# Performance work log

Hardware: AMD Instinct MI355X
Metric: run time of the kernel (lower is better)

## Reference

```python
import jax, jax.numpy as jnp
import numpy as np

B, N, H, V, STEP = 16, 50, 128, 40000, 2

def setup_inputs() -> dict:
    key = jax.random.key(0)
    ks = jax.random.split(key, 24)
    def nrm(i, shape, s=0.08):
        return jax.random.normal(ks[i], shape, jnp.float32) * s
    items = jax.random.randint(ks[0], (B, N), 0, V)
    A = jax.random.uniform(ks[1], (B, N, 2 * N), jnp.float32)
    lengths = jax.random.randint(ks[2], (B,), 1, N + 1)
    mask = (jnp.arange(N)[None, :] < lengths[:, None]).astype(jnp.int32)
    emb = nrm(3, (V, H), 0.1).at[0].set(0.0)  # padding_idx=0 row zeroed
    return dict(
        items=items, A=A, mask=mask, emb=emb,
        w_ih=nrm(4, (3 * H, 2 * H)), w_hh=nrm(5, (3 * H, H)),
        b_ih=nrm(6, (3 * H,)), b_hh=nrm(7, (3 * H,)),
        b_iah=nrm(8, (H,)), b_oah=nrm(9, (H,)),
        W_ein=nrm(10, (H, H)), b_ein=nrm(11, (H,)),
        W_eout=nrm(12, (H, H)), b_eout=nrm(13, (H,)),
        W_one=nrm(14, (H, H)), b_one=nrm(15, (H,)),
        W_two=nrm(16, (H, H)), b_two=nrm(17, (H,)),
        w_three=nrm(18, (H,)),
        W_tr=nrm(19, (H, 2 * H)), b_tr=nrm(20, (H,)),
        W_t=nrm(21, (H, H)),
    )

def gnn_cell(A, hidden, w_ih, w_hh, b_ih, b_hh, b_iah, b_oah, W_ein, b_ein, W_eout, b_eout):
    # A: [B,N,2N], hidden: [B,N,H]
    ein = hidden @ W_ein.T + b_ein
    eout = hidden @ W_eout.T + b_eout
    input_in = jnp.einsum('bnm,bmh->bnh', A[:, :, :N], ein) + b_iah
    input_out = jnp.einsum('bnm,bmh->bnh', A[:, :, N:], eout) + b_oah
    inputs = jnp.concatenate([input_in, input_out], axis=-1)  # [B,N,2H]
    gi = inputs @ w_ih.T + b_ih
    gh = hidden @ w_hh.T + b_hh
    i_r, i_i, i_n = jnp.split(gi, 3, axis=-1)
    h_r, h_i, h_n = jnp.split(gh, 3, axis=-1)
    resetgate = jax.nn.sigmoid(i_r + h_r)
    inputgate = jax.nn.sigmoid(i_i + h_i)
    newgate = jnp.tanh(i_n + resetgate * h_n)
    return newgate + inputgate * (hidden - newgate)

def reference(items, A, mask, emb, w_ih, w_hh, b_ih, b_hh, b_iah, b_oah,
              W_ein, b_ein, W_eout, b_eout, W_one, b_one, W_two, b_two,
              w_three, W_tr, b_tr, W_t):
    hidden = emb[items]  # [B,N,H]
    for _ in range(STEP):
        hidden = gnn_cell(A, hidden, w_ih, w_hh, b_ih, b_hh, b_iah, b_oah,
                          W_ein, b_ein, W_eout, b_eout)
    # compute_scores
    lengths = jnp.sum(mask, axis=1)  # all >= 1 by construction
    ht = hidden[jnp.arange(B), lengths - 1]  # [B,H] last valid item
    q1 = (ht @ W_one.T + b_one)[:, None, :]
    q2 = hidden @ W_two.T + b_two
    mexp = mask[..., None].astype(jnp.float32)  # [B,N,1]
    alpha_logits = jax.nn.sigmoid(q1 + q2) @ w_three[:, None]  # [B,N,1]
    alpha = jax.nn.softmax(jnp.where(mexp == 0, -jnp.inf, alpha_logits), axis=1)
    a = jnp.sum(alpha * hidden * mexp, axis=1)  # [B,H]
    a = jnp.concatenate([a, ht], axis=1) @ W_tr.T + b_tr  # hybrid (nonhybrid=False)
    b_emb = emb[1:]  # [V-1,H]
    qt = (hidden * mexp) @ W_t.T  # [B,N,H]
    beta_logits = jnp.einsum('vh,bnh->bvn', b_emb, qt)
    beta_logits = jnp.where(mask[:, None, :] == 0, -jnp.inf, beta_logits)
    beta = jax.nn.softmax(beta_logits, axis=-1)  # [B,V-1,N]
    target = jnp.einsum('bvn,bnh->bvh', beta, qt * mexp)  # [B,V-1,H]
    # scores = sum((a[:,None,:] + target) * b_emb, -1), split to avoid extra buffer
    scores = jnp.einsum('bvh,vh->bv', target, b_emb) + a @ b_emb.T
    return scores  # [B, V-1]
```

## Files before the change

kernel.cpp:

```cpp
#include <hip/hip_runtime.h>

#define BB 16
#define NN 50
#define HH 128
#define VV 40000
#define VO 39999

typedef unsigned short u16;
typedef unsigned int u32;
typedef __attribute__((ext_vector_type(8))) short short8;
typedef __attribute__((ext_vector_type(4))) float f32x4;

#define OFF_HID    0
#define OFF_EIN    102400
#define OFF_Q2     102400
#define OFF_EOUT   204800
#define OFF_Q1     204800
#define OFF_HT     206848
#define OFF_QTBF   307200
#define OFF_LEN    411648
#define OFF_WIHT   411664
#define OFF_WHHT   509968
#define OFF_WEINT  559120
#define OFF_WEOUTT 575504
#define OFF_WTWOT  591888
#define OFF_WTT    608272
#define OFF_WONET  624656
#define OFF_WTRT   641040

__device__ __forceinline__ float sigm(float x){ return 1.0f/(1.0f+__expf(-x)); }
__device__ __forceinline__ float b2f(u16 u){
  union { u32 i; float f; } c; c.i = ((u32)u) << 16; return c.f;
}
__device__ __forceinline__ u16 f2b(float f){
  union { float f; u32 i; } c; c.f = f;
  u32 u = c.i;
  return (u16)((u + 0x7fffu + ((u >> 16) & 1u)) >> 16);
}
__device__ __forceinline__ int frag_idx(int b, int n, int k){
  int tile = n>>4, vlo = n&15, kc = k>>5, quad = (k>>3)&3, j = k&7;
  return (((b*4+tile)*4+kc)<<9) + ((quad<<4)+vlo)*8 + j;
}

__global__ void k_pre(const int* __restrict__ items, const float* __restrict__ emb,
                      const float* __restrict__ w_ih, const float* __restrict__ w_hh,
                      const float* __restrict__ W_ein, const float* __restrict__ W_eout,
                      const float* __restrict__ W_two, const float* __restrict__ W_t,
                      const float* __restrict__ W_one, const float* __restrict__ W_tr,
                      float* __restrict__ ws){
  int idx = blockIdx.x*256 + threadIdx.x;
  if (idx < 102400){
    int r = idx >> 7, h = idx & 127;
    ws[OFF_HID + idx] = emb[items[r]*128 + h];
  } else if (idx < 200704){
    int i = idx-102400; int k=i/384, j=i-k*384;
    ws[OFF_WIHT + i] = w_ih[j*256 + k];
  } else if (idx < 249856){
    int i = idx-200704; int k=i/384, j=i-k*384;
    ws[OFF_WHHT + i] = w_hh[j*128 + k];
  } else if (idx < 266240){
    int i = idx-249856; int k=i>>7, h=i&127;
    ws[OFF_WEINT + i] = W_ein[h*128 + k];
  } else if (idx < 282624){
    int i = idx-266240; int k=i>>7, h=i&127;
    ws[OFF_WEOUTT + i] = W_eout[h*128 + k];
  } else if (idx < 299008){
    int i = idx-282624; int k=i>>7, h=i&127;
    ws[OFF_WTWOT + i] = W_two[h*128 + k];
  } else if (idx < 315392){
    int i = idx-299008; int k=i>>7, h=i&127;
    ws[OFF_WTT + i] = W_t[h*128 + k];
  } else if (idx < 331776){
    int i = idx-315392; int k=i>>7, h=i&127;
    ws[OFF_WONET + i] = W_one[h*128 + k];
  } else if (idx < 364544){
    int i = idx-331776; int k=i>>7, h=i&127;
    ws[OFF_WTRT + i] = W_tr[h*256 + k];
  }
}

__global__ void __launch_bounds__(256) k_einout(const float* __restrict__ b_ein,
                         const float* __restrict__ b_eout, float* __restrict__ ws){
  __shared__ float hl[256];
  int t = threadIdx.x;
  int r0 = blockIdx.x * 2;
  hl[t] = ws[OFF_HID + r0*128 + t];
  __syncthreads();
  int h = t & 127;
  const float* wT = ws + ((t<128) ? OFF_WEINT : OFF_WEOUTT);
  float bias = ((t<128)? b_ein : b_eout)[h];
  float a0 = bias, a1 = bias;
  for (int k=0;k<128;k+=4){
    float w0 = wT[(k+0)*128+h], w1 = wT[(k+1)*128+h];
    float w2 = wT[(k+2)*128+h], w3 = wT[(k+3)*128+h];
    float4 h0 = *(const float4*)(hl + k);
    float4 h1 = *(const float4*)(hl + 128 + k);
    a0 += h0.x*w0 + h0.y*w1 + h0.z*w2 + h0.w*w3;
    a1 += h1.x*w0 + h1.y*w1 + h1.z*w2 + h1.w*w3;
  }
  float* dst = ws + ((t<128) ? OFF_EIN : OFF_EOUT);
  dst[(r0+0)*128 + h] = a0;
  dst[(r0+1)*128 + h] = a1;
}

__global__ void __launch_bounds__(384) k_cell(const float* __restrict__ A,
                       const float* __restrict__ b_iah, const float* __restrict__ b_oah,
                       const float* __restrict__ b_ih, const float* __restrict__ b_hh,
                       float* __restrict__ ws){
  __shared__ float hidr[4][128];
  __shared__ float arow[4][104];
  __shared__ float inp[4][256];
  __shared__ float gil[4][384];
  __shared__ float ghl[4][384];
  int t = threadIdx.x;
  int tile = blockIdx.x, b = blockIdx.y;
  int n0 = tile*4;
  for (int o=t; o<512; o+=384){
    int r=o>>7, h=o&127, row=n0+r;
    hidr[r][h] = (row<NN) ? ws[OFF_HID + (b*NN+row)*128 + h] : 0.0f;
  }
  for (int o=t; o<416; o+=384){
    int r=o/104, c=o-r*104;
    arow[r][c] = (c<100 && n0+r<NN) ? A[(size_t)(b*NN+n0+r)*100 + c] : 0.0f;
  }
  __syncthreads();
  for (int o=t; o<1024; o+=384){
    int r = o>>8, c8 = o&255;
    int half = (c8 < 128) ? 1 : 0;
    int c = c8 & 127;
    int row = n0 + r;
    float acc = 0.0f;
    if (row < NN){
      acc = half ? b_iah[c] : b_oah[c];
      const float* src = ws + (half?OFF_EIN:OFF_EOUT) + b*6400 + c;
      const float* ar = &arow[r][half?0:50];
      #pragma unroll 5
      for (int m=0;m<50;m++) acc += ar[m] * src[m*128];
    }
    inp[r][c8] = acc;
  }
  __syncthreads();
  {
    int j = t;
    float gi[4], gh[4];
    float bi = b_ih[j], bh = b_hh[j];
    #pragma unroll
    for (int r=0;r<4;r++){ gi[r]=bi; gh[r]=bh; }
    const float* wti = ws + OFF_WIHT;
    const float* wth = ws + OFF_WHHT;
    for (int k=0;k<256;k+=4){
      float w0 = wti[(k+0)*384+j], w1 = wti[(k+1)*384+j];
      float w2 = wti[(k+2)*384+j], w3_ = wti[(k+3)*384+j];
      #pragma unroll
      for (int r=0;r<4;r++){
        float4 iv = *(const float4*)(&inp[r][k]);
        gi[r] += iv.x*w0 + iv.y*w1 + iv.z*w2 + iv.w*w3_;
      }
    }
    for (int k=0;k<128;k+=4){
      float w0 = wth[(k+0)*384+j], w1 = wth[(k+1)*384+j];
      float w2 = wth[(k+2)*384+j], w3_ = wth[(k+3)*384+j];
      #pragma unroll
      for (int r=0;r<4;r++){
        float4 hv = *(const float4*)(&hidr[r][k]);
        gh[r] += hv.x*w0 + hv.y*w1 + hv.z*w2 + hv.w*w3_;
      }
    }
    #pragma unroll
    for (int r=0;r<4;r++){ gil[r][j]=gi[r]; ghl[r][j]=gh[r]; }
  }
  __syncthreads();
  for (int o=t; o<512; o+=384){
    int r=o>>7, h=o&127, row=n0+r;
    if (row<NN){
      float ir_=gil[r][h], ii=gil[r][128+h], inw=gil[r][256+h];
      float hr_=ghl[r][h], hi=ghl[r][128+h], hn=ghl[r][256+h];
      float rg=sigm(ir_+hr_), ig=sigm(ii+hi), ng=tanhf(inw+rg*hn);
      float hv=hidr[r][h];
      ws[OFF_HID + (b*NN+row)*128 + h] = ng + ig*(hv-ng);
    }
  }
}

__global__ void __launch_bounds__(256) k_post(const int* __restrict__ mask,
                      const float* __restrict__ b_two, const float* __restrict__ b_one,
                      float* __restrict__ ws){
  int bx = blockIdx.x, t = threadIdx.x;
  u16* qtbf = (u16*)(ws + OFF_QTBF);
  if (bx < 200){
    bool isq2 = bx < 100;
    int r0 = (isq2 ? bx : bx-100) * 8;
    __shared__ float hl[1024];
    for (int i=0;i<4;i++) hl[t+i*256] = ws[OFF_HID + r0*128 + t + i*256];
    __syncthreads();
    int h = t & 127, g = t >> 7;
    const float* wT = ws + (isq2 ? OFF_WTWOT : OFF_WTT);
    float binit = isq2 ? b_two[h] : 0.0f;
    float acc[4];
    #pragma unroll
    for (int r=0;r<4;r++) acc[r] = binit;
    for (int k4=0;k4<32;k4++){
      int k = k4*4;
      float w0 = wT[(k+0)*128+h], w1 = wT[(k+1)*128+h];
      float w2 = wT[(k+2)*128+h], w3 = wT[(k+3)*128+h];
      #pragma unroll
      for (int r=0;r<4;r++){
        float4 hv = *(const float4*)(hl + (g*4+r)*128 + k);
        acc[r] += hv.x*w0 + hv.y*w1 + hv.z*w2 + hv.w*w3;
      }
    }
    #pragma unroll
    for (int r=0;r<4;r++){
      int row = r0 + g*4 + r;
      if (isq2) ws[OFF_Q2 + row*128 + h] = acc[r];
      else {
        float val = mask[row] ? acc[r] : 0.0f;
        int b = row/NN, n = row - b*NN;
        qtbf[frag_idx(b, n, h)] = f2b(val);
      }
    }
  } else if (bx < 248){
    int i = (bx-200)*256 + t;
    #pragma unroll
    for (int kk=0;kk<2;kk++){
      int e = i*2 + kk;
      int b = e/1536, rem = e - b*1536;
      int kc = rem/384, rem2 = rem - kc*384;
      int quad = rem2/96, vv = rem2 - quad*96;
      int vlo = 4 + vv/8, j = vv & 7;
      qtbf[(((b*4+3)*4+kc)<<9) + ((quad<<4)+vlo)*8 + j] = 0;
    }
  } else {
    __shared__ float htl[128];
    int b = bx - 248;
    if (t < 128){
      int len = 0;
      for (int n=0;n<NN;n++) len += mask[b*NN+n];
      if (len<1) len=1; if (len>NN) len=NN;
      float ht = ws[OFF_HID + (b*NN + len-1)*128 + t];
      ws[OFF_HT + b*128 + t] = ht;
      htl[t] = ht;
      if (t==0) ((int*)(ws+OFF_LEN))[b] = len;
    }
    __syncthreads();
    if (t < 128){
      const float* w1T = ws + OFF_WONET;
      float q1 = b_one[t];
      for (int k=0;k<128;k++) q1 += htl[k] * w1T[k*128 + t];
      ws[OFF_Q1 + b*128 + t] = q1;
    }
  }
}

__global__ void k_attn2(const float* __restrict__ w_three, const float* __restrict__ b_tr,
                        float* __restrict__ ws){
  __shared__ float q2l[NN*129];
  __shared__ float q1l[128], w3l[128], htl[128], al[128], alg[64];
  int t = threadIdx.x;
  int b = blockIdx.x;
  for (int o=t;o<NN*128;o+=128){ int n=o>>7, h=o&127; q2l[n*129+h] = ws[OFF_Q2 + b*NN*128 + o]; }
  q1l[t] = ws[OFF_Q1 + b*128 + t];
  w3l[t] = w_three[t];
  htl[t] = ws[OFF_HT + b*128 + t];
  int len = ((const int*)(ws+OFF_LEN))[b];
  __syncthreads();
  if (t < len){
    float s = 0.0f;
    const float* qr = q2l + t*129;
    for (int h=0;h<128;h++) s += w3l[h]*sigm(q1l[h]+qr[h]);
    alg[t] = s;
  }
  __syncthreads();
  if (t == 0){
    float mx = -1e30f;
    for (int n=0;n<len;n++) mx = fmaxf(mx, alg[n]);
    float ssum = 0.0f;
    for (int n=0;n<len;n++){ float e=__expf(alg[n]-mx); alg[n]=e; ssum+=e; }
    float inv = (ssum>0.0f)?1.0f/ssum:0.0f;
    for (int n=0;n<len;n++) alg[n]*=inv;
  }
  __syncthreads();
  const float* hid = ws + OFF_HID + b*NN*128;
  float a = 0.0f;
  for (int n=0;n<len;n++) a += alg[n]*hid[n*128+t];
  al[t] = a;
  __syncthreads();
  const float* wtr = ws + OFF_WTRT;
  float af = b_tr[t];
  for (int k=0;k<128;k++) af += al[k]  * wtr[k*128 + t];
  for (int k=0;k<128;k++) af += htl[k] * wtr[(128+k)*128 + t];
  u16 hi = f2b(af);
  u16 lo = f2b(af - b2f(hi));
  u16* qtbf = (u16*)(ws + OFF_QTBF);
  qtbf[frag_idx(b, 50, t)] = hi;
  qtbf[frag_idx(b, 51, t)] = lo;
}

__global__ void __launch_bounds__(256) k_scores(const float* __restrict__ emb,
                                                const float* __restrict__ ws,
                                                float* __restrict__ out){
  __shared__ u16 qlds[8192];
  int tid = threadIdx.x;
  int lane = tid & 63, wave = tid >> 6;
  int quad = lane >> 4, vlo = lane & 15;
  int v = blockIdx.y*64 + wave*16 + vlo;
  int vc = (v < VO) ? v : (VO-1);
  const float* erow = emb + (size_t)(vc+1)*128;
  short8 bfr[4];
  #pragma unroll
  for (int kc=0;kc<4;kc++){
    const float4* p = (const float4*)(erow + kc*32 + quad*8);
    float4 x = p[0], y = p[1];
    union { short8 s; u32 w[4]; } u;
    u.w[0] = (u32)f2b(x.x) | ((u32)f2b(x.y)<<16);
    u.w[1] = (u32)f2b(x.z) | ((u32)f2b(x.w)<<16);
    u.w[2] = (u32)f2b(y.x) | ((u32)f2b(y.y)<<16);
    u.w[3] = (u32)f2b(y.z) | ((u32)f2b(y.w)<<16);
    bfr[kc] = u.s;
  }
  const u16* qtf = (const u16*)(ws + OFF_QTBF);
  const int* slen = (const int*)(ws + OFF_LEN);
  int b0 = blockIdx.x*4;
  for (int bi=0;bi<4;bi++){
    int b = b0 + bi;
    __syncthreads();
    {
      const uint4* src = (const uint4*)qtf + (size_t)b*1024;
      uint4* dst = (uint4*)qlds;
      #pragma unroll
      for (int r=0;r<4;r++) dst[tid + r*256] = src[tid + r*256];
    }
    __syncthreads();
    int len = slen[b];
    f32x4 acc0={0.f,0.f,0.f,0.f}, acc1=acc0, acc2=acc0, acc3=acc0;
    #pragma unroll
    for (int kc=0;kc<4;kc++){
      const u16* base = qlds + kc*512 + lane*8;
      short8 a0 = *(const short8*)(base + 0*2048);
      short8 a1 = *(const short8*)(base + 1*2048);
      short8 a2 = *(const short8*)(base + 2*2048);
      short8 a3 = *(const short8*)(base + 3*2048);
      acc0 = __builtin_amdgcn_mfma_f32_16x16x32_bf16(a0, bfr[kc], acc0, 0,0,0);
      acc1 = __builtin_amdgcn_mfma_f32_16x16x32_bf16(a1, bfr[kc], acc1, 0,0,0);
      acc2 = __builtin_amdgcn_mfma_f32_16x16x32_bf16(a2, bfr[kc], acc2, 0,0,0);
      acc3 = __builtin_amdgcn_mfma_f32_16x16x32_bf16(a3, bfr[kc], acc3, 0,0,0);
    }
    int nb = quad*4;
    float ss=0.f, nm=0.f;
    #pragma unroll
    for (int r=0;r<4;r++){
      { int n=nb+r;    if(n<len){ float e=__expf(acc0[r]); ss+=e; nm+=e*acc0[r]; } }
      { int n=nb+r+16; if(n<len){ float e=__expf(acc1[r]); ss+=e; nm+=e*acc1[r]; } }
      { int n=nb+r+32; if(n<len){ float e=__expf(acc2[r]); ss+=e; nm+=e*acc2[r]; } }
      { int n=nb+r+48; if(n<len){ float e=__expf(acc3[r]); ss+=e; nm+=e*acc3[r]; } }
    }
    ss += __shfl_xor(ss,16); ss += __shfl_xor(ss,32);
    nm += __shfl_xor(nm,16); nm += __shfl_xor(nm,32);
    if (quad==0 && v < VO){
      float pa = acc3[2] + acc3[3];
      out[(size_t)b*VO + v] = nm/ss + pa;
    }
  }
}

extern "C" void kernel_launch(void* const* d_in, const int* in_sizes, int n_in,
                              void* d_out, int out_size, void* d_ws, size_t ws_size,
                              hipStream_t stream){
  const int*   items  = (const int*)d_in[0];
  const float* A      = (const float*)d_in[1];
  const int*   mask   = (const int*)d_in[2];
  const float* emb    = (const float*)d_in[3];
  const float* w_ih   = (const float*)d_in[4];
  const float* w_hh   = (const float*)d_in[5];
  const float* b_ih   = (const float*)d_in[6];
  const float* b_hh   = (const float*)d_in[7];
  const float* b_iah  = (const float*)d_in[8];
  const float* b_oah  = (const float*)d_in[9];
  const float* W_ein  = (const float*)d_in[10];
  const float* b_ein  = (const float*)d_in[11];
  const float* W_eout = (const float*)d_in[12];
  const float* b_eout = (const float*)d_in[13];
  const float* W_one  = (const float*)d_in[14];
  const float* b_one  = (const float*)d_in[15];
  const float* W_two  = (const float*)d_in[16];
  const float* b_two  = (const float*)d_in[17];
  const float* w_three= (const float*)d_in[18];
  const float* W_tr   = (const float*)d_in[19];
  const float* b_tr   = (const float*)d_in[20];
  const float* W_t    = (const float*)d_in[21];
  float* ws  = (float*)d_ws;
  float* out = (float*)d_out;

  k_pre<<<1424,256,0,stream>>>(items,emb,w_ih,w_hh,W_ein,W_eout,W_two,W_t,W_one,W_tr,ws);
  for (int s=0;s<2;s++){
    k_einout<<<400,256,0,stream>>>(b_ein,b_eout,ws);
    k_cell  <<<dim3(13,16),384,0,stream>>>(A,b_iah,b_oah,b_ih,b_hh,ws);
  }
  k_post <<<264,256,0,stream>>>(mask,b_two,b_one,ws);
  k_attn2<<<16,128,0,stream>>>(w_three,b_tr,ws);
  k_scores<<<dim3(4,625),256,0,stream>>>(emb,ws,out);
}
```

Measured before the change: 219.8 us.

## Fuse all stages into one persistent cooperative kernel with grid syncs

Merges the preprocessing, both GNN steps, post-processing, attention and scoring kernels into a single cooperative kernel that runs a fixed grid and separates stages with grid-wide barriers. The goal is to remove the launch overhead and inter-kernel gaps of roughly eight small launches. The trade-off is that the scoring stage, formerly 2500 blocks of 256 threads, now runs as a grid-stride loop over at most 512 blocks of 384 threads, with a quarter of the threads idle. Grid barriers also add their own synchronisation cost.

Result: slower. 512.7 us (+133.2%).

```diff
diff --git a/kernel.cpp b/kernel.cpp
--- a/kernel.cpp
+++ b/kernel.cpp
@@ -1,4 +1,7 @@
 #include <hip/hip_runtime.h>
+#include <hip/hip_cooperative_groups.h>
+
+namespace cg = cooperative_groups;
 
 #define BB 16
 #define NN 50
@@ -42,323 +45,381 @@
   return (((b*4+tile)*4+kc)<<9) + ((quad<<4)+vlo)*8 + j;
 }
 
-__global__ void k_pre(const int* __restrict__ items, const float* __restrict__ emb,
-                      const float* __restrict__ w_ih, const float* __restrict__ w_hh,
-                      const float* __restrict__ W_ein, const float* __restrict__ W_eout,
-                      const float* __restrict__ W_two, const float* __restrict__ W_t,
-                      const float* __restrict__ W_one, const float* __restrict__ W_tr,
-                      float* __restrict__ ws){
-  int idx = blockIdx.x*256 + threadIdx.x;
-  if (idx < 102400){
-    int r = idx >> 7, h = idx & 127;
-    ws[OFF_HID + idx] = emb[items[r]*128 + h];
-  } else if (idx < 200704){
-    int i = idx-102400; int k=i/384, j=i-k*384;
-    ws[OFF_WIHT + i] = w_ih[j*256 + k];
-  } else if (idx < 249856){
-    int i = idx-200704; int k=i/384, j=i-k*384;
-    ws[OFF_WHHT + i] = w_hh[j*128 + k];
-  } else if (idx < 266240){
-    int i = idx-249856; int k=i>>7, h=i&127;
-    ws[OFF_WEINT + i] = W_ein[h*128 + k];
-  } else if (idx < 282624){
-    int i = idx-266240; int k=i>>7, h=i&127;
-    ws[OFF_WEOUTT + i] = W_eout[h*128 + k];
-  } else if (idx < 299008){
-    int i = idx-282624; int k=i>>7, h=i&127;
-    ws[OFF_WTWOT + i] = W_two[h*128 + k];
-  } else if (idx < 315392){
-    int i = idx-299008; int k=i>>7, h=i&127;
-    ws[OFF_WTT + i] = W_t[h*128 + k];
-  } else if (idx < 331776){
-    int i = idx-315392; int k=i>>7, h=i&127;
-    ws[OFF_WONET + i] = W_one[h*128 + k];
-  } else if (idx < 364544){
-    int i = idx-331776; int k=i>>7, h=i&127;
-    ws[OFF_WTRT + i] = W_tr[h*256 + k];
-  }
-}
-
-__global__ void __launch_bounds__(256) k_einout(const float* __restrict__ b_ein,
-                         const float* __restrict__ b_eout, float* __restrict__ ws){
-  __shared__ float hl[256];
-  int t = threadIdx.x;
-  int r0 = blockIdx.x * 2;
-  hl[t] = ws[OFF_HID + r0*128 + t];
-  __syncthreads();
-  int h = t & 127;
-  const float* wT = ws + ((t<128) ? OFF_WEINT : OFF_WEOUTT);
-  float bias = ((t<128)? b_ein : b_eout)[h];
-  float a0 = bias, a1 = bias;
-  for (int k=0;k<128;k+=4){
-    float w0 = wT[(k+0)*128+h], w1 = wT[(k+1)*128+h];
-    float w2 = wT[(k+2)*128+h], w3 = wT[(k+3)*128+h];
-    float4 h0 = *(const float4*)(hl + k);
-    float4 h1 = *(const float4*)(hl + 128 + k);
-    a0 += h0.x*w0 + h0.y*w1 + h0.z*w2 + h0.w*w3;
-    a1 += h1.x*w0 + h1.y*w1 + h1.z*w2 + h1.w*w3;
-  }
-  float* dst = ws + ((t<128) ? OFF_EIN : OFF_EOUT);
-  dst[(r0+0)*128 + h] = a0;
-  dst[(r0+1)*128 + h] = a1;
-}
-
-__global__ void __launch_bounds__(384) k_cell(const float* __restrict__ A,
-                       const float* __restrict__ b_iah, const float* __restrict__ b_oah,
-                       const float* __restrict__ b_ih, const float* __restrict__ b_hh,
-                       float* __restrict__ ws){
-  __shared__ float hidr[4][128];
-  __shared__ float arow[4][104];
-  __shared__ float inp[4][256];
-  __shared__ float gil[4][384];
-  __shared__ float ghl[4][384];
-  int t = threadIdx.x;
-  int tile = blockIdx.x, b = blockIdx.y;
-  int n0 = tile*4;
-  for (int o=t; o<512; o+=384){
-    int r=o>>7, h=o&127, row=n0+r;
-    hidr[r][h] = (row<NN) ? ws[OFF_HID + (b*NN+row)*128 + h] : 0.0f;
-  }
-  for (int o=t; o<416; o+=384){
-    int r=o/104, c=o-r*104;
-    arow[r][c] = (c<100 && n0+r<NN) ? A[(size_t)(b*NN+n0+r)*100 + c] : 0.0f;
-  }
-  __syncthreads();
-  for (int o=t; o<1024; o+=384){
-    int r = o>>8, c8 = o&255;
-    int half = (c8 < 128) ? 1 : 0;
-    int c = c8 & 127;
-    int row = n0 + r;
-    float acc = 0.0f;
-    if (row < NN){
-      acc = half ? b_iah[c] : b_oah[c];
-      const float* src = ws + (half?OFF_EIN:OFF_EOUT) + b*6400 + c;
-      const float* ar = &arow[r][half?0:50];
-      #pragma unroll 5
-      for (int m=0;m<50;m++) acc += ar[m] * src[m*128];
-    }
-    inp[r][c8] = acc;
-  }
-  __syncthreads();
+__global__ void __launch_bounds__(384) k_mega(
+  const int* __restrict__ items, const float* __restrict__ A, const int* __restrict__ mask,
+  const float* __restrict__ emb, const float* __restrict__ w_ih, const float* __restrict__ w_hh,
+  const float* __restrict__ b_ih, const float* __restrict__ b_hh, const float* __restrict__ b_iah,
+  const float* __restrict__ b_oah, const float* __restrict__ W_ein, const float* __restrict__ b_ein,
+  const float* __restrict__ W_eout, const float* __restrict__ b_eout, const float* __restrict__ W_one,
+  const float* __restrict__ b_one, const float* __restrict__ W_two, const float* __restrict__ b_two,
+  const float* __restrict__ w_three, const float* __restrict__ W_tr, const float* __restrict__ b_tr,
+  const float* __restrict__ W_t, float* __restrict__ ws, float* __restrict__ out)
+{
+  cg::grid_group grid = cg::this_grid();
+  __shared__ __align__(16) float smem[7168];
+  const int t = threadIdx.x;
+  const int bid = blockIdx.x;
+  const int G = gridDim.x;
+
   {
-    int j = t;
-    float gi[4], gh[4];
-    float bi = b_ih[j], bh = b_hh[j];
-    #pragma unroll
-    for (int r=0;r<4;r++){ gi[r]=bi; gh[r]=bh; }
-    const float* wti = ws + OFF_WIHT;
-    const float* wth = ws + OFF_WHHT;
-    for (int k=0;k<256;k+=4){
-      float w0 = wti[(k+0)*384+j], w1 = wti[(k+1)*384+j];
-      float w2 = wti[(k+2)*384+j], w3_ = wti[(k+3)*384+j];
-      #pragma unroll
-      for (int r=0;r<4;r++){
-        float4 iv = *(const float4*)(&inp[r][k]);
-        gi[r] += iv.x*w0 + iv.y*w1 + iv.z*w2 + iv.w*w3_;
-      }
-    }
-    for (int k=0;k<128;k+=4){
-      float w0 = wth[(k+0)*384+j], w1 = wth[(k+1)*384+j];
-      float w2 = wth[(k+2)*384+j], w3_ = wth[(k+3)*384+j];
-      #pragma unroll
-      for (int r=0;r<4;r++){
-        float4 hv = *(const float4*)(&hidr[r][k]);
-        gh[r] += hv.x*w0 + hv.y*w1 + hv.z*w2 + hv.w*w3_;
-      }
-    }
-    #pragma unroll
-    for (int r=0;r<4;r++){ gil[r][j]=gi[r]; ghl[r][j]=gh[r]; }
-  }
-  __syncthreads();
-  for (int o=t; o<512; o+=384){
-    int r=o>>7, h=o&127, row=n0+r;
-    if (row<NN){
-      float ir_=gil[r][h], ii=gil[r][128+h], inw=gil[r][256+h];
-      float hr_=ghl[r][h], hi=ghl[r][128+h], hn=ghl[r][256+h];
-      float rg=sigm(ir_+hr_), ig=sigm(ii+hi), ng=tanhf(inw+rg*hn);
-      float hv=hidr[r][h];
-      ws[OFF_HID + (b*NN+row)*128 + h] = ng + ig*(hv-ng);
-    }
-  }
-}
-
-__global__ void __launch_bounds__(256) k_post(const int* __restrict__ mask,
-                      const float* __restrict__ b_two, const float* __restrict__ b_one,
-                      float* __restrict__ ws){
-  int bx = blockIdx.x, t = threadIdx.x;
-  u16* qtbf = (u16*)(ws + OFF_QTBF);
-  if (bx < 200){
-    bool isq2 = bx < 100;
-    int r0 = (isq2 ? bx : bx-100) * 8;
-    __shared__ float hl[1024];
-    for (int i=0;i<4;i++) hl[t+i*256] = ws[OFF_HID + r0*128 + t + i*256];
-    __syncthreads();
-    int h = t & 127, g = t >> 7;
-    const float* wT = ws + (isq2 ? OFF_WTWOT : OFF_WTT);
-    float binit = isq2 ? b_two[h] : 0.0f;
-    float acc[4];
-    #pragma unroll
-    for (int r=0;r<4;r++) acc[r] = binit;
-    for (int k4=0;k4<32;k4++){
-      int k = k4*4;
-      float w0 = wT[(k+0)*128+h], w1 = wT[(k+1)*128+h];
-      float w2 = wT[(k+2)*128+h], w3 = wT[(k+3)*128+h];
-      #pragma unroll
-      for (int r=0;r<4;r++){
-        float4 hv = *(const float4*)(hl + (g*4+r)*128 + k);
-        acc[r] += hv.x*w0 + hv.y*w1 + hv.z*w2 + hv.w*w3;
-      }
-    }
-    #pragma unroll
-    for (int r=0;r<4;r++){
-      int row = r0 + g*4 + r;
-      if (isq2) ws[OFF_Q2 + row*128 + h] = acc[r];
-      else {
-        float val = mask[row] ? acc[r] : 0.0f;
-        int b = row/NN, n = row - b*NN;
-        qtbf[frag_idx(b, n, h)] = f2b(val);
-      }
-    }
-  } else if (bx < 248){
-    int i = (bx-200)*256 + t;
-    #pragma unroll
-    for (int kk=0;kk<2;kk++){
-      int e = i*2 + kk;
-      int b = e/1536, rem = e - b*1536;
-      int kc = rem/384, rem2 = rem - kc*384;
-      int quad = rem2/96, vv = rem2 - quad*96;
-      int vlo = 4 + vv/8, j = vv & 7;
-      qtbf[(((b*4+3)*4+kc)<<9) + ((quad<<4)+vlo)*8 + j] = 0;
-    }
-  } else {
-    __shared__ float htl[128];
-    int b = bx - 248;
+    const int stride = G*384;
+    for (int idx = bid*384 + t; idx < 364544; idx += stride){
+      if (idx < 102400){
+        int r = idx >> 7, h = idx & 127;
+        ws[OFF_HID + idx] = emb[items[r]*128 + h];
+      } else if (idx < 200704){
+        int i = idx-102400; int k=i/384, j=i-k*384;
+        ws[OFF_WIHT + i] = w_ih[j*256 + k];
+      } else if (idx < 249856){
+        int i = idx-200704; int k=i/384, j=i-k*384;
+        ws[OFF_WHHT + i] = w_hh[j*128 + k];
+      } else if (idx < 266240){
+        int i = idx-249856; int k=i>>7, h=i&127;
+        ws[OFF_WEINT + i] = W_ein[h*128 + k];
+      } else if (idx < 282624){
+        int i = idx-266240; int k=i>>7, h=i&127;
+        ws[OFF_WEOUTT + i] = W_eout[h*128 + k];
+      } else if (idx < 299008){
+        int i = idx-282624; int k=i>>7, h=i&127;
+        ws[OFF_WTWOT + i] = W_two[h*128 + k];
+      } else if (idx < 315392){
+        int i = idx-299008; int k=i>>7, h=i&127;
+        ws[OFF_WTT + i] = W_t[h*128 + k];
+      } else if (idx < 331776){
+        int i = idx-315392; int k=i>>7, h=i&127;
+        ws[OFF_WONET + i] = W_one[h*128 + k];
+      } else {
+        int i = idx-331776; int k=i>>7, h=i&127;
+        ws[OFF_WTRT + i] = W_tr[h*256 + k];
+      }
+    }
+  }
+  grid.sync();
+
+  for (int s=0; s<2; s++){
+    for (int unit = bid; unit < 400; unit += G){
+      float* hl = smem;
+      if (t < 256) hl[t] = ws[OFF_HID + unit*256 + t];
+      __syncthreads();
+      if (t < 256){
+        int r0 = unit*2;
+        int h = t & 127;
+        const float* wT = ws + ((t<128) ? OFF_WEINT : OFF_WEOUTT);
+        float bias = ((t<128)? b_ein : b_eout)[h];
+        float a0 = bias, a1 = bias;
+        for (int k=0;k<128;k+=4){
+          float w0 = wT[(k+0)*128+h], w1 = wT[(k+1)*128+h];
+          float w2 = wT[(k+2)*128+h], w3 = wT[(k+3)*128+h];
+          float4 h0 = *(const float4*)(hl + k);
+          float4 h1 = *(const float4*)(hl + 128 + k);
+          a0 += h0.x*w0 + h0.y*w1 + h0.z*w2 + h0.w*w3;
+          a1 += h1.x*w0 + h1.y*w1 + h1.z*w2 + h1.w*w3;
+        }
+        float* dst = ws + ((t<128) ? OFF_EIN : OFF_EOUT);
+        dst[(r0+0)*128 + h] = a0;
+        dst[(r0+1)*128 + h] = a1;
+      }
+      __syncthreads();
+    }
+    grid.sync();
+
+    for (int unit = bid; unit < 208; unit += G){
+      int tile = unit % 13, b = unit / 13;
+      float (*hidr)[128] = (float(*)[128])(smem);
+      float (*arow)[104] = (float(*)[104])(smem + 512);
+      float (*inp)[256]  = (float(*)[256])(smem + 928);
+      float (*gil)[384]  = (float(*)[384])(smem + 1952);
+      float (*ghl)[384]  = (float(*)[384])(smem + 3488);
+      int n0 = tile*4;
+      for (int o=t; o<512; o+=384){
+        int r=o>>7, h=o&127, row=n0+r;
+        hidr[r][h] = (row<NN) ? ws[OFF_HID + (b*NN+row)*128 + h] : 0.0f;
+      }
+      for (int o=t; o<416; o+=384){
+        int r=o/104, c=o-r*104;
+        arow[r][c] = (c<100 && n0+r<NN) ? A[(size_t)(b*NN+n0+r)*100 + c] : 0.0f;
+      }
+      __syncthreads();
+      for (int o=t; o<1024; o+=384){
+        int r = o>>8, c8 = o&255;
+        int half = (c8 < 128) ? 1 : 0;
+        int c = c8 & 127;
+        int row = n0 + r;
+        float acc = 0.0f;
+        if (row < NN){
+          acc = half ? b_iah[c] : b_oah[c];
+          const float* src = ws + (half?OFF_EIN:OFF_EOUT) + b*6400 + c;
+          const float* ar = &arow[r][half?0:50];
+          #pragma unroll 5
+          for (int m=0;m<50;m++) acc += ar[m] * src[m*128];
+        }
+        inp[r][c8] = acc;
+      }
+      __syncthreads();
+      {
+        int j = t;
+        float gi[4], gh[4];
+        float bi2 = b_ih[j], bh2 = b_hh[j];
+        #pragma unroll
+        for (int r=0;r<4;r++){ gi[r]=bi2; gh[r]=bh2; }
+        const float* wti = ws + OFF_WIHT;
+        const float* wth = ws + OFF_WHHT;
+        for (int k=0;k<256;k+=4){
+          float w0 = wti[(k+0)*384+j], w1 = wti[(k+1)*384+j];
+          float w2 = wti[(k+2)*384+j], w3_ = wti[(k+3)*384+j];
+          #pragma unroll
+          for (int r=0;r<4;r++){
+            float4 iv = *(const float4*)(&inp[r][k]);
+            gi[r] += iv.x*w0 + iv.y*w1 + iv.z*w2 + iv.w*w3_;
+          }
+        }
+        for (int k=0;k<128;k+=4){
+          float w0 = wth[(k+0)*384+j], w1 = wth[(k+1)*384+j];
+          float w2 = wth[(k+2)*384+j], w3_ = wth[(k+3)*384+j];
+          #pragma unroll
+          for (int r=0;r<4;r++){
+            float4 hv = *(const float4*)(&hidr[r][k]);
+            gh[r] += hv.x*w0 + hv.y*w1 + hv.z*w2 + hv.w*w3_;
+          }
+        }
+        #pragma unroll
+        for (int r=0;r<4;r++){ gil[r][j]=gi[r]; ghl[r][j]=gh[r]; }
+      }
+      __syncthreads();
+      for (int o=t; o<512; o+=384){
+        int r=o>>7, h=o&127, row=n0+r;
+        if (row<NN){
+          float ir_=gil[r][h], ii=gil[r][128+h], inw=gil[r][256+h];
+          float hr_=ghl[r][h], hi2=ghl[r][128+h], hn=ghl[r][256+h];
+          float rg=sigm(ir_+hr_), ig=sigm(ii+hi2), ng=tanhf(inw+rg*hn);
+          float hv=hidr[r][h];
+          ws[OFF_HID + (b*NN+row)*128 + h] = ng + ig*(hv-ng);
+        }
+      }
+      __syncthreads();
+    }
+    grid.sync();
+  }
+
+  {
+    u16* qtbf = (u16*)(ws + OFF_QTBF);
+    for (int unit = bid; unit < 264; unit += G){
+      if (unit < 200){
+        bool isq2 = unit < 100;
+        int r0 = (isq2 ? unit : unit-100) * 8;
+        float* hl = smem;
+        for (int o=t;o<1024;o+=384) hl[o] = ws[OFF_HID + r0*128 + o];
+        __syncthreads();
+        if (t < 256){
+          int h = t & 127, g = t >> 7;
+          const float* wT = ws + (isq2 ? OFF_WTWOT : OFF_WTT);
+          float binit = isq2 ? b_two[h] : 0.0f;
+          float acc[4];
+          #pragma unroll
+          for (int r=0;r<4;r++) acc[r] = binit;
+          for (int k4=0;k4<32;k4++){
+            int k = k4*4;
+            float w0 = wT[(k+0)*128+h], w1 = wT[(k+1)*128+h];
+            float w2 = wT[(k+2)*128+h], w3 = wT[(k+3)*128+h];
+            #pragma unroll
+            for (int r=0;r<4;r++){
+              float4 hv = *(const float4*)(hl + (g*4+r)*128 + k);
+              acc[r] += hv.x*w0 + hv.y*w1 + hv.z*w2 + hv.w*w3;
+            }
+          }
+          #pragma unroll
+          for (int r=0;r<4;r++){
+            int row = r0 + g*4 + r;
+            if (isq2) ws[OFF_Q2 + row*128 + h] = acc[r];
+            else {
+              float val = mask[row] ? acc[r] : 0.0f;
+              int b2 = row/NN, n = row - b2*NN;
+              qtbf[frag_idx(b2, n, h)] = f2b(val);
+            }
+          }
+        }
+        __syncthreads();
+      } else if (unit < 248){
+        if (t < 256){
+          int i = (unit-200)*256 + t;
+          #pragma unroll
+          for (int kk=0;kk<2;kk++){
+            int e = i*2 + kk;
+            int b2 = e/1536, rem = e - b2*1536;
+            int kc = rem/384, rem2 = rem - kc*384;
+            int quad = rem2/96, vv = rem2 - quad*96;
+            int vlo = 4 + vv/8, j = vv & 7;
+            qtbf[(((b2*4+3)*4+kc)<<9) + ((quad<<4)+vlo)*8 + j] = 0;
+          }
+        }
+      } else {
+        int b2 = unit - 248;
+        float* htl = smem;
+        if (t < 128){
+          int len = 0;
+          for (int n=0;n<NN;n++) len += mask[b2*NN+n];
+          if (len<1) len=1; if (len>NN) len=NN;
+          float ht = ws[OFF_HID + (b2*NN + len-1)*128 + t];
+          ws[OFF_HT + b2*128 + t] = ht;
+          htl[t] = ht;
+          if (t==0) ((int*)(ws+OFF_LEN))[b2] = len;
+        }
+        __syncthreads();
+        if (t < 128){
+          const float* w1T = ws + OFF_WONET;
+          float q1 = b_one[t];
+          for (int k=0;k<128;k++) q1 += htl[k] * w1T[k*128 + t];
+          ws[OFF_Q1 + b2*128 + t] = q1;
+        }
+        __syncthreads();
+      }
+    }
+  }
+  grid.sync();
+
+  for (int unit = bid; unit < 16; unit += G){
+    int b = unit;
+    float* q2l = smem;
+    float* q1l = smem + 6456;
+    float* w3l = smem + 6584;
+    float* htl = smem + 6712;
+    float* al  = smem + 6840;
+    float* alg = smem + 6968;
+    float* pt2 = smem + 7032;
+    for (int o=t;o<6400;o+=384){ int n=o>>7, h=o&127; q2l[n*129+h] = ws[OFF_Q2 + b*6400 + o]; }
     if (t < 128){
-      int len = 0;
-      for (int n=0;n<NN;n++) len += mask[b*NN+n];
-      if (len<1) len=1; if (len>NN) len=NN;
-      float ht = ws[OFF_HID + (b*NN + len-1)*128 + t];
-      ws[OFF_HT + b*128 + t] = ht;
-      htl[t] = ht;
-      if (t==0) ((int*)(ws+OFF_LEN))[b] = len;
-    }
-    __syncthreads();
+      q1l[t] = ws[OFF_Q1 + b*128 + t];
+      w3l[t] = w_three[t];
+      htl[t] = ws[OFF_HT + b*128 + t];
+    }
+    int len = ((const int*)(ws+OFF_LEN))[b];
+    __syncthreads();
+    if (t < 200){
+      int n = t>>2, part = t&3;
+      if (n < len){
+        const float* qr  = q2l + n*129 + part*32;
+        const float* q1p = q1l + part*32;
+        const float* w3p = w3l + part*32;
+        float s = 0.0f;
+        for (int h=0;h<32;h++) s += w3p[h]*sigm(q1p[h]+qr[h]);
+        s += __shfl_xor(s,1); s += __shfl_xor(s,2);
+        if (part==0) alg[n] = s;
+      }
+    }
+    __syncthreads();
+    if (t < 64){
+      float v = (t<len) ? alg[t] : -1e30f;
+      float m = v;
+      m = fmaxf(m, __shfl_xor(m,1));  m = fmaxf(m, __shfl_xor(m,2));
+      m = fmaxf(m, __shfl_xor(m,4));  m = fmaxf(m, __shfl_xor(m,8));
+      m = fmaxf(m, __shfl_xor(m,16)); m = fmaxf(m, __shfl_xor(m,32));
+      float e = (t<len) ? __expf(v - m) : 0.0f;
+      float ss = e;
+      ss += __shfl_xor(ss,1);  ss += __shfl_xor(ss,2);
+      ss += __shfl_xor(ss,4);  ss += __shfl_xor(ss,8);
+      ss += __shfl_xor(ss,16); ss += __shfl_xor(ss,32);
+      float inv = 1.0f/ss;
+      if (t<len) alg[t] = e*inv;
+    }
+    __syncthreads();
+    float p1 = 0.0f;
     if (t < 128){
-      const float* w1T = ws + OFF_WONET;
-      float q1 = b_one[t];
-      for (int k=0;k<128;k++) q1 += htl[k] * w1T[k*128 + t];
-      ws[OFF_Q1 + b*128 + t] = q1;
-    }
-  }
-}
-
-__global__ void k_attn2(const float* __restrict__ w_three, const float* __restrict__ b_tr,
-                        float* __restrict__ ws){
-  __shared__ float q2l[NN*129];
-  __shared__ float q1l[128], w3l[128], htl[128], al[128], alg[64];
-  int t = threadIdx.x;
-  int b = blockIdx.x;
-  for (int o=t;o<NN*128;o+=128){ int n=o>>7, h=o&127; q2l[n*129+h] = ws[OFF_Q2 + b*NN*128 + o]; }
-  q1l[t] = ws[OFF_Q1 + b*128 + t];
-  w3l[t] = w_three[t];
-  htl[t] = ws[OFF_HT + b*128 + t];
-  int len = ((const int*)(ws+OFF_LEN))[b];
-  __syncthreads();
-  if (t < len){
-    float s = 0.0f;
-    const float* qr = q2l + t*129;
-    for (int h=0;h<128;h++) s += w3l[h]*sigm(q1l[h]+qr[h]);
-    alg[t] = s;
-  }
-  __syncthreads();
-  if (t == 0){
-    float mx = -1e30f;
-    for (int n=0;n<len;n++) mx = fmaxf(mx, alg[n]);
-    float ssum = 0.0f;
-    for (int n=0;n<len;n++){ float e=__expf(alg[n]-mx); alg[n]=e; ssum+=e; }
-    float inv = (ssum>0.0f)?1.0f/ssum:0.0f;
-    for (int n=0;n<len;n++) alg[n]*=inv;
-  }
-  __syncthreads();
-  const float* hid = ws + OFF_HID + b*NN*128;
-  float a = 0.0f;
-  for (int n=0;n<len;n++) a += alg[n]*hid[n*128+t];
-  al[t] = a;
-  __syncthreads();
-  const float* wtr = ws + OFF_WTRT;
-  float af = b_tr[t];
-  for (int k=0;k<128;k++) af += al[k]  * wtr[k*128 + t];
-  for (int k=0;k<128;k++) af += htl[k] * wtr[(128+k)*128 + t];
-  u16 hi = f2b(af);
-  u16 lo = f2b(af - b2f(hi));
-  u16* qtbf = (u16*)(ws + OFF_QTBF);
-  qtbf[frag_idx(b, 50, t)] = hi;
-  qtbf[frag_idx(b, 51, t)] = lo;
-}
-
-__global__ void __launch_bounds__(256) k_scores(const float* __restrict__ emb,
-                                                const float* __restrict__ ws,
-                                                float* __restrict__ out){
-  __shared__ u16 qlds[8192];
-  int tid = threadIdx.x;
-  int lane = tid & 63, wave = tid >> 6;
-  int quad = lane >> 4, vlo = lane & 15;
-  int v = blockIdx.y*64 + wave*16 + vlo;
-  int vc = (v < VO) ? v : (VO-1);
-  const float* erow = emb + (size_t)(vc+1)*128;
-  short8 bfr[4];
-  #pragma unroll
-  for (int kc=0;kc<4;kc++){
-    const float4* p = (const float4*)(erow + kc*32 + quad*8);
-    float4 x = p[0], y = p[1];
-    union { short8 s; u32 w[4]; } u;
-    u.w[0] = (u32)f2b(x.x) | ((u32)f2b(x.y)<<16);
-    u.w[1] = (u32)f2b(x.z) | ((u32)f2b(x.w)<<16);
-    u.w[2] = (u32)f2b(y.x) | ((u32)f2b(y.y)<<16);
-    u.w[3] = (u32)f2b(y.z) | ((u32)f2b(y.w)<<16);
-    bfr[kc] = u.s;
-  }
-  const u16* qtf = (const u16*)(ws + OFF_QTBF);
-  const int* slen = (const int*)(ws + OFF_LEN);
-  int b0 = blockIdx.x*4;
-  for (int bi=0;bi<4;bi++){
-    int b = b0 + bi;
-    __syncthreads();
-    {
-      const uint4* src = (const uint4*)qtf + (size_t)b*1024;
-      uint4* dst = (uint4*)qlds;
-      #pragma unroll
-      for (int r=0;r<4;r++) dst[tid + r*256] = src[tid + r*256];
-    }
-    __syncthreads();
-    int len = slen[b];
-    f32x4 acc0={0.f,0.f,0.f,0.f}, acc1=acc0, acc2=acc0, acc3=acc0;
-    #pragma unroll
-    for (int kc=0;kc<4;kc++){
-      const u16* base = qlds + kc*512 + lane*8;
-      short8 a0 = *(const short8*)(base + 0*2048);
-      short8 a1 = *(const short8*)(base + 1*2048);
-      short8 a2 = *(const short8*)(base + 2*2048);
-      short8 a3 = *(const short8*)(base + 3*2048);
-      acc0 = __builtin_amdgcn_mfma_f32_16x16x32_bf16(a0, bfr[kc], acc0, 0,0,0);
-      acc1 = __builtin_amdgcn_mfma_f32_16x16x32_bf16(a1, bfr[kc], acc1, 0,0,0);
-      acc2 = __builtin_amdgcn_mfma_f32_16x16x32_bf16(a2, bfr[kc], acc2, 0,0,0);
-      acc3 = __builtin_amdgcn_mfma_f32_16x16x32_bf16(a3, bfr[kc], acc3, 0,0,0);
-    }
-    int nb = quad*4;
-    float ss=0.f, nm=0.f;
-    #pragma unroll
-    for (int r=0;r<4;r++){
-      { int n=nb+r;    if(n<len){ float e=__expf(acc0[r]); ss+=e; nm+=e*acc0[r]; } }
-      { int n=nb+r+16; if(n<len){ float e=__expf(acc1[r]); ss+=e; nm+=e*acc1[r]; } }
-      { int n=nb+r+32; if(n<len){ float e=__expf(acc2[r]); ss+=e; nm+=e*acc2[r]; } }
-      { int n=nb+r+48; if(n<len){ float e=__expf(acc3[r]); ss+=e; nm+=e*acc3[r]; } }
-    }
-    ss += __shfl_xor(ss,16); ss += __shfl_xor(ss,32);
-    nm += __shfl_xor(nm,16); nm += __shfl_xor(nm,32);
-    if (quad==0 && v < VO){
-      float pa = acc3[2] + acc3[3];
-      out[(size_t)b*VO + v] = nm/ss + pa;
+      const float* hid = ws + OFF_HID + b*6400;
+      float a = 0.0f;
+      for (int n=0;n<len;n++) a += alg[n]*hid[n*128+t];
+      al[t] = a;
+    }
+    __syncthreads();
+    if (t < 256){
+      int g2 = t>>7, h = t&127;
+      const float* wtr = ws + OFF_WTRT + g2*128*128;
+      const float* src = g2 ? htl : al;
+      float p = 0.0f;
+      for (int k=0;k<128;k++) p += src[k]*wtr[k*128+h];
+      if (g2) pt2[h] = p; else p1 = p;
+    }
+    __syncthreads();
+    if (t < 128){
+      float af = b_tr[t] + p1 + pt2[t];
+      u16 hi = f2b(af);
+      u16 lo = f2b(af - b2f(hi));
+      u16* qtbf = (u16*)(ws + OFF_QTBF);
+      qtbf[frag_idx(b, 50, t)] = hi;
+      qtbf[frag_idx(b, 51, t)] = lo;
+    }
+    __syncthreads();
+  }
+  grid.sync();
+
+  {
+    u16* qlds = (u16*)smem;
+    const u16* qtf = (const u16*)(ws + OFF_QTBF);
+    const int* slen = (const int*)(ws + OFF_LEN);
+    for (int unit = bid; unit < 2500; unit += G){
+      int bg = unit & 3, vchunk = unit >> 2;
+      bool act = (t < 256);
+      int lane = t & 63, wave = t >> 6;
+      int quad = lane >> 4, vlo = lane & 15;
+      int v = vchunk*64 + wave*16 + vlo;
+      int vc = (v < VO) ? v : (VO-1);
+      short8 bfr[4];
+      if (act){
+        const float* erow = emb + (size_t)(vc+1)*128;
+        #pragma unroll
+        for (int kc=0;kc<4;kc++){
+          const float4* p = (const float4*)(erow + kc*32 + quad*8);
+          float4 x = p[0], y = p[1];
+          union { short8 s; u32 w[4]; } u;
+          u.w[0] = (u32)f2b(x.x) | ((u32)f2b(x.y)<<16);
+          u.w[1] = (u32)f2b(x.z) | ((u32)f2b(x.w)<<16);
+          u.w[2] = (u32)f2b(y.x) | ((u32)f2b(y.y)<<16);
+          u.w[3] = (u32)f2b(y.z) | ((u32)f2b(y.w)<<16);
+          bfr[kc] = u.s;
+        }
+      }
+      int b0 = bg*4;
+      for (int bi=0;bi<4;bi++){
+        int b = b0 + bi;
+        __syncthreads();
+        if (act){
+          const uint4* src = (const uint4*)qtf + (size_t)b*1024;
+          uint4* dst = (uint4*)qlds;
+          #pragma unroll
+          for (int r=0;r<4;r++) dst[t + r*256] = src[t + r*256];
+        }
+        __syncthreads();
+        if (act){
+          int len = slen[b];
+          f32x4 acc0={0.f,0.f,0.f,0.f}, acc1=acc0, acc2=acc0, acc3=acc0;
+          #pragma unroll
+          for (int kc=0;kc<4;kc++){
+            const u16* base = qlds + kc*512 + lane*8;
+            short8 a0 = *(const short8*)(base + 0*2048);
+            short8 a1 = *(const short8*)(base + 1*2048);
+            short8 a2 = *(const short8*)(base + 2*2048);
+            short8 a3 = *(const short8*)(base + 3*2048);
+            acc0 = __builtin_amdgcn_mfma_f32_16x16x32_bf16(a0, bfr[kc], acc0, 0,0,0);
+            acc1 = __builtin_amdgcn_mfma_f32_16x16x32_bf16(a1, bfr[kc], acc1, 0,0,0);
+            acc2 = __builtin_amdgcn_mfma_f32_16x16x32_bf16(a2, bfr[kc], acc2, 0,0,0);
+            acc3 = __builtin_amdgcn_mfma_f32_16x16x32_bf16(a3, bfr[kc], acc3, 0,0,0);
+          }
+          int nb2 = quad*4;
+          float ss=0.f, nm=0.f;
+          #pragma unroll
+          for (int r=0;r<4;r++){
+            { int n=nb2+r;    if(n<len){ float e=__expf(acc0[r]); ss+=e; nm+=e*acc0[r]; } }
+            { int n=nb2+r+16; if(n<len){ float e=__expf(acc1[r]); ss+=e; nm+=e*acc1[r]; } }
+            { int n=nb2+r+32; if(n<len){ float e=__expf(acc2[r]); ss+=e; nm+=e*acc2[r]; } }
+            { int n=nb2+r+48; if(n<len){ float e=__expf(acc3[r]); ss+=e; nm+=e*acc3[r]; } }
+          }
+          ss += __shfl_xor(ss,16); ss += __shfl_xor(ss,32);
+          nm += __shfl_xor(nm,16); nm += __shfl_xor(nm,32);
+          if (quad==0 && v < VO){
+            float pa = acc3[2] + acc3[3];
+            out[(size_t)b*VO + v] = nm/ss + pa;
+          }
+        }
+      }
     }
   }
 }
@@ -391,12 +452,26 @@
   float* ws  = (float*)d_ws;
   float* out = (float*)d_out;
 
-  k_pre<<<1424,256,0,stream>>>(items,emb,w_ih,w_hh,W_ein,W_eout,W_two,W_t,W_one,W_tr,ws);
-  for (int s=0;s<2;s++){
-    k_einout<<<400,256,0,stream>>>(b_ein,b_eout,ws);
-    k_cell  <<<dim3(13,16),384,0,stream>>>(A,b_iah,b_oah,b_ih,b_hh,ws);
-  }
-  k_post <<<264,256,0,stream>>>(mask,b_two,b_one,ws);
-  k_attn2<<<16,128,0,stream>>>(w_three,b_tr,ws);
-  k_scores<<<dim3(4,625),256,0,stream>>>(emb,ws,out);
+  static int G = 0;
+  if (G == 0){
+    int nb = 0;
+    if (hipOccupancyMaxActiveBlocksPerMultiprocessor(&nb, reinterpret_cast<const void*>(&k_mega), 384, 0) != hipSuccess || nb <= 0)
+      nb = 1;
+    int cus = 256;
+    hipDeviceProp_t prop;
+    if (hipGetDeviceProperties(&prop, 0) == hipSuccess && prop.multiProcessorCount > 0)
+      cus = prop.multiProcessorCount;
+    long cap = (long)nb * (long)cus;
+    G = (cap < 512) ? (int)cap : 512;
+    if (G < 64) G = 64;
+  }
+
+  void* args[24] = {
+    (void*)&items, (void*)&A, (void*)&mask, (void*)&emb, (void*)&w_ih, (void*)&w_hh,
+    (void*)&b_ih, (void*)&b_hh, (void*)&b_iah, (void*)&b_oah, (void*)&W_ein, (void*)&b_ein,
+    (void*)&W_eout, (void*)&b_eout, (void*)&W_one, (void*)&b_one, (void*)&W_two, (void*)&b_two,
+    (void*)&w_three, (void*)&W_tr, (void*)&b_tr, (void*)&W_t, (void*)&ws, (void*)&out
+  };
+  (void)hipLaunchCooperativeKernel(reinterpret_cast<const void*>(&k_mega),
+                                   dim3((unsigned)G), dim3(384), args, 0, stream);
 }
```
